# Kernel optimization log

Hardware: AMD Instinct MI355X
Metric: run time of the kernel (lower is better)

The kernel has to match this reference:

```python
import jax, jax.numpy as jnp
import numpy as np

C_Z = 128
N_HEADS = 4
HEAD_DIM = 32
TOTAL = N_HEADS * HEAD_DIM
B, N = 1, 256


def setup_inputs() -> dict:
    key = jax.random.key(0)
    ks = jax.random.split(key, 10)
    s = lambda k, sh: jax.random.normal(k, sh, dtype=jnp.float32) * 0.02
    return {
        "pair_representation": jax.random.normal(ks[0], (B, N, N, C_Z), dtype=jnp.float32),
        "ln_gamma": jnp.ones((C_Z,), jnp.float32),
        "ln_beta": jnp.zeros((C_Z,), jnp.float32),
        "Wq": s(ks[1], (C_Z, TOTAL)),
        "Wk": s(ks[2], (C_Z, TOTAL)),
        "Wv": s(ks[3], (C_Z, TOTAL)),
        "Wb": s(ks[4], (C_Z, N_HEADS)),
        "Wg": s(ks[5], (C_Z, TOTAL)),
        "bg": jnp.zeros((TOTAL,), jnp.float32),
        "Wo": s(ks[6], (TOTAL, C_Z)),
        "bo": jnp.zeros((C_Z,), jnp.float32),
    }


def reference(pair_representation, ln_gamma, ln_beta, Wq, Wk, Wv, Wb, Wg, bg, Wo, bo):
    x = pair_representation
    # LayerNorm over c_z
    mu = jnp.mean(x, axis=-1, keepdims=True)
    var = jnp.mean((x - mu) ** 2, axis=-1, keepdims=True)
    x = (x - mu) * jax.lax.rsqrt(var + 1e-5) * ln_gamma + ln_beta

    b, n, _, _ = x.shape
    split = lambda t: t.reshape(b, n, n, N_HEADS, HEAD_DIM)
    Q = split(x @ Wq)  # [b,i,j,h,d]
    K = split(x @ Wk)
    V = split(x @ Wv)
    G = jax.nn.sigmoid(split(x @ Wg + bg))
    Bias = x @ Wb  # [b,j,k,h]

    scores = jnp.einsum("bijhd,bikhd->bijkh", Q, K) / np.float32(np.sqrt(HEAD_DIM))
    scores = scores + Bias[:, None]  # broadcast over i
    attn = jax.nn.softmax(scores, axis=3)  # over k
    vals = jnp.einsum("bijkh,bikhd->bijhd", attn, V)
    vals = (G * vals).reshape(b, n, n, TOTAL)
    return vals @ Wo + bo
```

## Files before the change

### kernel.cpp

```cpp
#include <hip/hip_runtime.h>
#include <hip/hip_bf16.h>


#define QSCALE 0.17677669529663687f

typedef __attribute__((ext_vector_type(8))) short bf16x8;
typedef __attribute__((ext_vector_type(4))) short bf16x4;
typedef __attribute__((ext_vector_type(4))) float f32x4;

#define MFMA32(a, b, c) __builtin_amdgcn_mfma_f32_16x16x32_bf16((a), (b), (c), 0, 0, 0)

__device__ __forceinline__ f32x4 mfma16_asm(bf16x4 a, bf16x4 b, f32x4 c) {
    f32x4 d;
    asm volatile("v_mfma_f32_16x16x16_bf16 %0, %1, %2, %3"
                 : "=v"(d) : "v"(a), "v"(b), "v"(c));
    return d;
}

#if !defined(__HIP_DEVICE_COMPILE__)
#define MFMA16(a, b, c) (c)
#elif __has_builtin(__builtin_amdgcn_mfma_f32_16x16x16bf16_1k)
#define MFMA16(a, b, c) __builtin_amdgcn_mfma_f32_16x16x16bf16_1k((a), (b), (c), 0, 0, 0)
#else
#define MFMA16(a, b, c) mfma16_asm((a), (b), (c))
#endif

__device__ __forceinline__ ushort f2bf(float f) {
    uint32_t u = __builtin_bit_cast(uint32_t, f);
    uint32_t r = (u + 0x7FFFu + ((u >> 16) & 1u)) >> 16;
    return (ushort)r;
}
__device__ __forceinline__ uint pk2(float a, float b) {
    union { __hip_bfloat162 h; uint u; } cv;
    cv.h = __float22bfloat162_rn(make_float2(a, b));
    return cv.u;
}

__global__ __launch_bounds__(256) void prep_bias_kernel(
    const float* __restrict__ Wq, const float* __restrict__ Wk, const float* __restrict__ Wv,
    const float* __restrict__ Wg, const float* __restrict__ Wo, const float* __restrict__ Wb,
    const float* __restrict__ x, const float* __restrict__ gamma, const float* __restrict__ beta,
    ushort* __restrict__ Wfrag, ushort* __restrict__ WoFrag,
    ushort* __restrict__ xn, float* __restrict__ EbF)
{
    __shared__ float WbS[512];
    __shared__ float gS[128];
    __shared__ float bS[128];

    if (blockIdx.x < 320) {
        int idx = blockIdx.x * 256 + threadIdx.x;
        if (idx < 65536) {
            int j = idx & 7, lane = (idx >> 3) & 63, ks = (idx >> 9) & 3, ct = idx >> 11;
            int n = ct * 16 + (lane & 15);
            int k = ks * 32 + (lane >> 4) * 8 + j;
            float v;
            if (n < 128)      v = Wq[k * 128 + n] * QSCALE;
            else if (n < 256) v = Wk[k * 128 + (n - 128)];
            else if (n < 384) v = Wv[k * 128 + (n - 256)];
            else              v = Wg[k * 128 + (n - 384)];
            Wfrag[idx] = f2bf(v);
        } else {
            int idx2 = idx - 65536;
            int j = idx2 & 7, lane = (idx2 >> 3) & 63, ks = (idx2 >> 9) & 3, ct = idx2 >> 11;
            int n = ct * 16 + (lane & 15);
            int k = ks * 32 + (lane >> 4) * 8 + j;
            WoFrag[idx2] = f2bf(Wo[k * 128 + n]);
        }
        return;
    }

    const int t = threadIdx.x;
    if (t < 128)      { *(f32x4*)&WbS[t * 4] = *(const f32x4*)(Wb + t * 4); }
    else if (t < 160) { int c = (t - 128) * 4; *(f32x4*)&gS[c] = *(const f32x4*)(gamma + c); }
    else if (t < 192) { int c = (t - 160) * 4; *(f32x4*)&bS[c] = *(const f32x4*)(beta + c); }
    __syncthreads();

    const int wave = t >> 6, lane = t & 63, m = lane & 15, quad = lane >> 4;
    const int p = (blockIdx.x - 320) * 64 + wave * 16 + m;

    const float* rp0 = x + (size_t)p * 128;
    f32x4 xa[4][2];
    float sum = 0.f, ssq = 0.f;
#pragma unroll
    for (int ks = 0; ks < 4; ++ks) {
        xa[ks][0] = *(const f32x4*)(rp0 + ks * 32 + quad * 8);
        xa[ks][1] = *(const f32x4*)(rp0 + ks * 32 + quad * 8 + 4);
#pragma unroll
        for (int q4 = 0; q4 < 2; ++q4) {
            f32x4 v = xa[ks][q4];
            sum += v[0] + v[1] + v[2] + v[3];
            ssq += v[0]*v[0] + v[1]*v[1] + v[2]*v[2] + v[3]*v[3];
        }
    }
    sum += __shfl_xor(sum, 16); ssq += __shfl_xor(ssq, 16);
    sum += __shfl_xor(sum, 32); ssq += __shfl_xor(ssq, 32);
    const float mu   = sum * (1.f / 128.f);
    const float rstd = rsqrtf(ssq * (1.f / 128.f) - mu * mu + 1e-5f);

    float b0 = 0.f, b1 = 0.f, b2 = 0.f, b3 = 0.f;
#pragma unroll
    for (int ks = 0; ks < 4; ++ks) {
        uint4 pkd;
        uint pw[4];
#pragma unroll
        for (int q4 = 0; q4 < 2; ++q4) {
            const int c = ks * 32 + quad * 8 + q4 * 4;
            f32x4 v = xa[ks][q4];
            float n0 = (v[0] - mu) * rstd * gS[c + 0] + bS[c + 0];
            float n1 = (v[1] - mu) * rstd * gS[c + 1] + bS[c + 1];
            float n2 = (v[2] - mu) * rstd * gS[c + 2] + bS[c + 2];
            float n3 = (v[3] - mu) * rstd * gS[c + 3] + bS[c + 3];
            pw[q4 * 2]     = pk2(n0, n1);
            pw[q4 * 2 + 1] = pk2(n2, n3);
            f32x4 w0 = *(const f32x4*)&WbS[(c + 0) * 4];
            f32x4 w1 = *(const f32x4*)&WbS[(c + 1) * 4];
            f32x4 w2 = *(const f32x4*)&WbS[(c + 2) * 4];
            f32x4 w3 = *(const f32x4*)&WbS[(c + 3) * 4];
            b0 += n0*w0[0] + n1*w1[0] + n2*w2[0] + n3*w3[0];
            b1 += n0*w0[1] + n1*w1[1] + n2*w2[1] + n3*w3[1];
            b2 += n0*w0[2] + n1*w1[2] + n2*w2[2] + n3*w3[2];
            b3 += n0*w0[3] + n1*w1[3] + n2*w2[3] + n3*w3[3];
        }
        pkd.x = pw[0]; pkd.y = pw[1]; pkd.z = pw[2]; pkd.w = pw[3];
        *(uint4*)(xn + (size_t)p * 128 + ks * 32 + quad * 8) = pkd;
    }
    b0 += __shfl_xor(b0, 16); b1 += __shfl_xor(b1, 16); b2 += __shfl_xor(b2, 16); b3 += __shfl_xor(b3, 16);
    b0 += __shfl_xor(b0, 32); b1 += __shfl_xor(b1, 32); b2 += __shfl_xor(b2, 32); b3 += __shfl_xor(b3, 32);

    if (quad == 0) {
        const int row = p >> 8, col = p & 255;
        float bb[4] = {b0, b1, b2, b3};
#pragma unroll
        for (int r = 0; r < 4; ++r) {
            int addr = (((r * 16 + (row >> 4)) * 16 + (col >> 4)) * 64 +
                        ((col & 15) >> 2) * 16 + (row & 15)) * 4 + (col & 3);
            EbF[addr] = __expf(bb[r]);
        }
    }
}

__global__ __launch_bounds__(512, 1) void fused_kernel(
    const ushort* __restrict__ xn, const ushort* __restrict__ Wfrag,
    const float* __restrict__ bg, const float* __restrict__ EbF,
    const ushort* __restrict__ WoFrag, const float* __restrict__ bo,
    float* __restrict__ out)
{
    extern __shared__ __align__(16) ushort SM[];
    ushort* KL = SM;
    ushort* VT = SM + 32768;

    const f32x4 ZERO4 = {0.f, 0.f, 0.f, 0.f};

    const int t = threadIdx.x;
    const int w = t >> 6, lane = t & 63, m = lane & 15, quad = lane >> 4;
    const int i = blockIdx.x;
    const int h = w >> 1, half = w & 1;
    const int jbase = half * 128;
    const ushort* xb = xn + ((size_t)i << 15);

    {
        const ushort* Wm = Wfrag + (h * 2) * 2048;
        bf16x8 wfr[2][4];
#pragma unroll
        for (int ctl = 0; ctl < 2; ++ctl)
#pragma unroll
            for (int ks = 0; ks < 4; ++ks)
                wfr[ctl][ks] = *(const bf16x8*)(Wm + ctl * 2048 + ks * 512 + lane * 8);
#pragma unroll
        for (int grp = 0; grp < 8; ++grp) {
            const int jloc = grp * 16 + m;
            bf16x8 xg[4];
            const ushort* xp = xb + (size_t)(jbase + jloc) * 128 + quad * 8;
#pragma unroll
            for (int ks = 0; ks < 4; ++ks) xg[ks] = *(const bf16x8*)(xp + ks * 32);
#pragma unroll
            for (int ctl = 0; ctl < 2; ++ctl) {
                f32x4 acc = ZERO4;
#pragma unroll
                for (int ks = 0; ks < 4; ++ks) acc = MFMA32(wfr[ctl][ks], xg[ks], acc);
                const int c = ctl * 16 + quad * 4;
                const int idx = (w * 4096 + jloc * 32 + c) ^ ((jloc & 3) << 3);
                uint2 u; u.x = pk2(acc[0], acc[1]); u.y = pk2(acc[2], acc[3]);
                *(uint2*)(KL + idx) = u;
            }
        }
    }
    bf16x8 qf[8];
#pragma unroll
    for (int jt = 0; jt < 8; ++jt) {
        const int jloc = jt * 16 + m;
        const int idx = (w * 4096 + jloc * 32 + quad * 8) ^ ((jloc & 3) << 3);
        qf[jt] = *(const bf16x8*)(KL + idx);
    }
    asm volatile("" ::: "memory");

    {
        const ushort* Wm = Wfrag + (8 + h * 2) * 2048;
        bf16x8 wfr[2][4];
#pragma unroll
        for (int ctl = 0; ctl < 2; ++ctl)
#pragma unroll
            for (int ks = 0; ks < 4; ++ks)
                wfr[ctl][ks] = *(const bf16x8*)(Wm + ctl * 2048 + ks * 512 + lane * 8);
#pragma unroll
        for (int grp = 0; grp < 8; ++grp) {
            const int k = jbase + grp * 16 + m;
            bf16x8 xg[4];
            const ushort* xp = xb + (size_t)k * 128 + quad * 8;
#pragma unroll
            for (int ks = 0; ks < 4; ++ks) xg[ks] = *(const bf16x8*)(xp + ks * 32);
#pragma unroll
            for (int ctl = 0; ctl < 2; ++ctl) {
                f32x4 acc = ZERO4;
#pragma unroll
                for (int ks = 0; ks < 4; ++ks) acc = MFMA32(wfr[ctl][ks], xg[ks], acc);
                const int d0 = ctl * 16 + quad * 4;
                const int idx = (h * 8192 + (k >> 1) * 64 + (k & 1) * 32 + d0) ^ (((k >> 1) & 7) << 3);
                uint2 u; u.x = pk2(acc[0], acc[1]); u.y = pk2(acc[2], acc[3]);
                *(uint2*)(KL + idx) = u;
            }
        }
    }

    {
        const ushort* Wm = Wfrag + (16 + h * 2) * 2048;
        bf16x8 wfr[2][4];
#pragma unroll
        for (int ctl = 0; ctl < 2; ++ctl)
#pragma unroll
            for (int ks = 0; ks < 4; ++ks)
                wfr[ctl][ks] = *(const bf16x8*)(Wm + ctl * 2048 + ks * 512 + lane * 8);
#pragma unroll
        for (int grp = 0; grp < 8; ++grp) {
            const int k = jbase + grp * 16 + m;
            bf16x8 xg[4];
            const ushort* xp = xb + (size_t)k * 128 + quad * 8;
#pragma unroll
            for (int ks = 0; ks < 4; ++ks) xg[ks] = *(const bf16x8*)(xp + ks * 32);
#pragma unroll
            for (int ctl = 0; ctl < 2; ++ctl) {
                f32x4 acc = ZERO4;
#pragma unroll
                for (int ks = 0; ks < 4; ++ks) acc = MFMA32(wfr[ctl][ks], xg[ks], acc);
#pragma unroll
                for (int r = 0; r < 4; ++r) {
                    const int d = ctl * 16 + quad * 4 + r;
                    const int idx = ((h * 32 + d) * 256 + k) ^ ((d & 7) << 3);
                    VT[idx] = f2bf(acc[r]);
                }
            }
        }
    }
    __syncthreads();

    f32x4 O[8][2];
    float lsum[8];
#pragma unroll
    for (int jt = 0; jt < 8; ++jt) {
        O[jt][0] = ZERO4;
        O[jt][1] = ZERO4;
        lsum[jt] = 0.f;
    }
    const float* ebB = EbF + ((size_t)(h * 16 + half * 8) << 12) + (lane << 2);

    for (int kh = 0; kh < 16; ++kh) {
        f32x4 eb[8];
#pragma unroll
        for (int jt = 0; jt < 8; ++jt)
            eb[jt] = *(const f32x4*)(ebB + (jt << 12) + (kh << 8));
        const int k = kh * 16 + m;
        const int kidx = (h * 8192 + (k >> 1) * 64 + (k & 1) * 32 + quad * 8) ^ (((k >> 1) & 7) << 3);
        bf16x8 kf = *(const bf16x8*)(KL + kidx);
        bf16x4 vf[2];
#pragma unroll
        for (int dt = 0; dt < 2; ++dt) {
            const int d = dt * 16 + m;
            const int vidx = ((h * 32 + d) * 256 + kh * 16 + quad * 4) ^ ((d & 7) << 3);
            uint2 vv = *(const uint2*)(VT + vidx);
            vf[dt] = __builtin_bit_cast(bf16x4, vv);
        }
#pragma unroll
        for (int jt = 0; jt < 8; ++jt) {
            f32x4 S = MFMA32(kf, qf[jt], ZERO4);
            float p0 = __expf(S[0]) * eb[jt][0];
            float p1 = __expf(S[1]) * eb[jt][1];
            float p2 = __expf(S[2]) * eb[jt][2];
            float p3 = __expf(S[3]) * eb[jt][3];
            lsum[jt] += p0 + p1 + p2 + p3;
            uint2 pu; pu.x = pk2(p0, p1); pu.y = pk2(p2, p3);
            bf16x4 pf = __builtin_bit_cast(bf16x4, pu);
#pragma unroll
            for (int dt = 0; dt < 2; ++dt)
                O[jt][dt] = MFMA16(vf[dt], pf, O[jt][dt]);
        }
    }

#pragma unroll
    for (int jt = 0; jt < 8; ++jt) {
        float s = lsum[jt];
        s += __shfl_xor(s, 16);
        s += __shfl_xor(s, 32);
        lsum[jt] = 1.f / s;
    }

    uint2 gva[8][2];
    {
        const ushort* Wm = Wfrag + (24 + h * 2) * 2048;
        bf16x8 wfr[2][4];
        f32x4 bg4[2];
#pragma unroll
        for (int ctl = 0; ctl < 2; ++ctl) {
#pragma unroll
            for (int ks = 0; ks < 4; ++ks)
                wfr[ctl][ks] = *(const bf16x8*)(Wm + ctl * 2048 + ks * 512 + lane * 8);
            bg4[ctl] = *(const f32x4*)(bg + h * 32 + ctl * 16 + quad * 4);
        }
#pragma unroll
        for (int grp = 0; grp < 8; ++grp) {
            const float rl = lsum[grp];
            bf16x8 xg[4];
            const ushort* xp = xb + (size_t)(jbase + grp * 16 + m) * 128 + quad * 8;
#pragma unroll
            for (int ks = 0; ks < 4; ++ks) xg[ks] = *(const bf16x8*)(xp + ks * 32);
#pragma unroll
            for (int ctl = 0; ctl < 2; ++ctl) {
                f32x4 acc = ZERO4;
#pragma unroll
                for (int ks = 0; ks < 4; ++ks) acc = MFMA32(wfr[ctl][ks], xg[ks], acc);
                float g0 = 1.f / (1.f + __expf(-(acc[0] + bg4[ctl][0])));
                float g1 = 1.f / (1.f + __expf(-(acc[1] + bg4[ctl][1])));
                float g2 = 1.f / (1.f + __expf(-(acc[2] + bg4[ctl][2])));
                float g3 = 1.f / (1.f + __expf(-(acc[3] + bg4[ctl][3])));
                float v0 = O[grp][ctl][0] * rl * g0;
                float v1 = O[grp][ctl][1] * rl * g1;
                float v2 = O[grp][ctl][2] * rl * g2;
                float v3 = O[grp][ctl][3] * rl * g3;
                gva[grp][ctl].x = pk2(v0, v1);
                gva[grp][ctl].y = pk2(v2, v3);
            }
        }
    }
    __syncthreads();

#pragma unroll
    for (int grp = 0; grp < 8; ++grp) {
        const int j = jbase + grp * 16 + m;
#pragma unroll
        for (int ctl = 0; ctl < 2; ++ctl) {
            const int c0 = h * 32 + ctl * 16 + quad * 4;
            const int idx = (j * 128 + c0) ^ ((j & 7) << 3);
            *(uint2*)(KL + idx) = gva[grp][ctl];
        }
    }
    __syncthreads();

    bf16x8 gf[2][4];
#pragma unroll
    for (int grp = 0; grp < 2; ++grp) {
        const int pl = w * 32 + grp * 16 + m;
#pragma unroll
        for (int ks = 0; ks < 4; ++ks) {
            const int idx = (pl * 128 + ks * 32 + quad * 8) ^ ((pl & 7) << 3);
            gf[grp][ks] = *(const bf16x8*)(KL + idx);
        }
    }
#pragma unroll
    for (int ct = 0; ct < 8; ++ct) {
        bf16x8 wfr[4];
#pragma unroll
        for (int ks = 0; ks < 4; ++ks)
            wfr[ks] = *(const bf16x8*)(WoFrag + (ct * 4 + ks) * 512 + lane * 8);
        const int c0 = ct * 16 + quad * 4;
        f32x4 bov = *(const f32x4*)(bo + c0);
#pragma unroll
        for (int grp = 0; grp < 2; ++grp) {
            f32x4 acc = ZERO4;
#pragma unroll
            for (int ks = 0; ks < 4; ++ks) acc = MFMA32(wfr[ks], gf[grp][ks], acc);
            const int p = i * 256 + w * 32 + grp * 16 + m;
            float4 v = make_float4(acc[0] + bov[0], acc[1] + bov[1],
                                   acc[2] + bov[2], acc[3] + bov[3]);
            *(float4*)(out + (size_t)p * 128 + c0) = v;
        }
    }
}

extern "C" void kernel_launch(void* const* d_in, const int* in_sizes, int n_in,
                              void* d_out, int out_size, void* d_ws, size_t ws_size,
                              hipStream_t stream) {
    const float* x     = (const float*)d_in[0];
    const float* gamma = (const float*)d_in[1];
    const float* beta  = (const float*)d_in[2];
    const float* Wq    = (const float*)d_in[3];
    const float* Wk    = (const float*)d_in[4];
    const float* Wv    = (const float*)d_in[5];
    const float* Wb    = (const float*)d_in[6];
    const float* Wg    = (const float*)d_in[7];
    const float* bg    = (const float*)d_in[8];
    const float* Wo    = (const float*)d_in[9];
    const float* bo    = (const float*)d_in[10];

    ushort* ws      = (ushort*)d_ws;
    ushort* Wfrag   = ws;
    ushort* WoFragp = ws + 65536;
    ushort* xn      = ws + 81920;
    float*  EbF     = (float*)(ws + 81920 + 8388608);

    static bool attr_set = false;
    if (!attr_set) {
        (void)hipFuncSetAttribute((const void*)fused_kernel,
                                  hipFuncAttributeMaxDynamicSharedMemorySize, 131072);
        attr_set = true;
    }

    prep_bias_kernel<<<1344, 256, 0, stream>>>(Wq, Wk, Wv, Wg, Wo, Wb,
                                               x, gamma, beta,
                                               Wfrag, WoFragp, xn, EbF);
    fused_kernel<<<256, 512, 131072, stream>>>(xn, Wfrag, bg, EbF,
                                               WoFragp, bo, (float*)d_out);
}
```

Measured before the change: 162.5 us.

## Split fused attention block across 16 waves with quarter-row j tiles and prefetch bias

Doubles the block to 1024 threads so each head is handled by four waves covering 64 j-rows each instead of two waves covering 128. Per-wave register state (Q fragments, O accumulators, sums) is halved, and the exp(bias) tiles are software-prefetched one k-step ahead. The aim is more latency hiding and wave-level parallelism per CU. In exchange, each wave repeats the K/V fragment loads over fewer j-rows, and the launch bound (1024, 4) caps registers per thread.

```diff
diff --git a/kernel.cpp b/kernel.cpp
--- a/kernel.cpp
+++ b/kernel.cpp
@@ -139,7 +139,7 @@
     }
 }
 
-__global__ __launch_bounds__(512, 1) void fused_kernel(
+__global__ __launch_bounds__(1024, 4) void fused_kernel(
     const ushort* __restrict__ xn, const ushort* __restrict__ Wfrag,
     const float* __restrict__ bg, const float* __restrict__ EbF,
     const ushort* __restrict__ WoFrag, const float* __restrict__ bo,
@@ -154,8 +154,9 @@
     const int t = threadIdx.x;
     const int w = t >> 6, lane = t & 63, m = lane & 15, quad = lane >> 4;
     const int i = blockIdx.x;
-    const int h = w >> 1, half = w & 1;
-    const int jbase = half * 128;
+    const int h = w >> 2, quarter = w & 3;
+    const int jbase = quarter * 64;
+    const int qreg = h * 8192 + quarter * 2048;
     const ushort* xb = xn + ((size_t)i << 15);
 
     {
@@ -167,7 +168,7 @@
             for (int ks = 0; ks < 4; ++ks)
                 wfr[ctl][ks] = *(const bf16x8*)(Wm + ctl * 2048 + ks * 512 + lane * 8);
 #pragma unroll
-        for (int grp = 0; grp < 8; ++grp) {
+        for (int grp = 0; grp < 4; ++grp) {
             const int jloc = grp * 16 + m;
             bf16x8 xg[4];
             const ushort* xp = xb + (size_t)(jbase + jloc) * 128 + quad * 8;
@@ -179,17 +180,17 @@
 #pragma unroll
                 for (int ks = 0; ks < 4; ++ks) acc = MFMA32(wfr[ctl][ks], xg[ks], acc);
                 const int c = ctl * 16 + quad * 4;
-                const int idx = (w * 4096 + jloc * 32 + c) ^ ((jloc & 3) << 3);
+                const int idx = (qreg + jloc * 32 + c) ^ ((jloc & 3) << 3);
                 uint2 u; u.x = pk2(acc[0], acc[1]); u.y = pk2(acc[2], acc[3]);
                 *(uint2*)(KL + idx) = u;
             }
         }
     }
-    bf16x8 qf[8];
-#pragma unroll
-    for (int jt = 0; jt < 8; ++jt) {
+    bf16x8 qf[4];
+#pragma unroll
+    for (int jt = 0; jt < 4; ++jt) {
         const int jloc = jt * 16 + m;
-        const int idx = (w * 4096 + jloc * 32 + quad * 8) ^ ((jloc & 3) << 3);
+        const int idx = (qreg + jloc * 32 + quad * 8) ^ ((jloc & 3) << 3);
         qf[jt] = *(const bf16x8*)(KL + idx);
     }
     asm volatile("" ::: "memory");
@@ -203,7 +204,7 @@
             for (int ks = 0; ks < 4; ++ks)
                 wfr[ctl][ks] = *(const bf16x8*)(Wm + ctl * 2048 + ks * 512 + lane * 8);
 #pragma unroll
-        for (int grp = 0; grp < 8; ++grp) {
+        for (int grp = 0; grp < 4; ++grp) {
             const int k = jbase + grp * 16 + m;
             bf16x8 xg[4];
             const ushort* xp = xb + (size_t)k * 128 + quad * 8;
@@ -231,7 +232,7 @@
             for (int ks = 0; ks < 4; ++ks)
                 wfr[ctl][ks] = *(const bf16x8*)(Wm + ctl * 2048 + ks * 512 + lane * 8);
 #pragma unroll
-        for (int grp = 0; grp < 8; ++grp) {
+        for (int grp = 0; grp < 4; ++grp) {
             const int k = jbase + grp * 16 + m;
             bf16x8 xg[4];
             const ushort* xp = xb + (size_t)k * 128 + quad * 8;
@@ -253,21 +254,26 @@
     }
     __syncthreads();
 
-    f32x4 O[8][2];
-    float lsum[8];
-#pragma unroll
-    for (int jt = 0; jt < 8; ++jt) {
+    f32x4 O[4][2];
+    float lsum[4];
+#pragma unroll
+    for (int jt = 0; jt < 4; ++jt) {
         O[jt][0] = ZERO4;
         O[jt][1] = ZERO4;
         lsum[jt] = 0.f;
     }
-    const float* ebB = EbF + ((size_t)(h * 16 + half * 8) << 12) + (lane << 2);
+    const float* ebB = EbF + ((size_t)(h * 16 + quarter * 4) << 12) + (lane << 2);
+
+    f32x4 ebc[4], ebn[4];
+#pragma unroll
+    for (int jt = 0; jt < 4; ++jt) ebc[jt] = *(const f32x4*)(ebB + (jt << 12));
 
     for (int kh = 0; kh < 16; ++kh) {
-        f32x4 eb[8];
-#pragma unroll
-        for (int jt = 0; jt < 8; ++jt)
-            eb[jt] = *(const f32x4*)(ebB + (jt << 12) + (kh << 8));
+        if (kh < 15) {
+#pragma unroll
+            for (int jt = 0; jt < 4; ++jt)
+                ebn[jt] = *(const f32x4*)(ebB + (jt << 12) + ((kh + 1) << 8));
+        }
         const int k = kh * 16 + m;
         const int kidx = (h * 8192 + (k >> 1) * 64 + (k & 1) * 32 + quad * 8) ^ (((k >> 1) & 7) << 3);
         bf16x8 kf = *(const bf16x8*)(KL + kidx);
@@ -280,12 +286,12 @@
             vf[dt] = __builtin_bit_cast(bf16x4, vv);
         }
 #pragma unroll
-        for (int jt = 0; jt < 8; ++jt) {
+        for (int jt = 0; jt < 4; ++jt) {
             f32x4 S = MFMA32(kf, qf[jt], ZERO4);
-            float p0 = __expf(S[0]) * eb[jt][0];
-            float p1 = __expf(S[1]) * eb[jt][1];
-            float p2 = __expf(S[2]) * eb[jt][2];
-            float p3 = __expf(S[3]) * eb[jt][3];
+            float p0 = __expf(S[0]) * ebc[jt][0];
+            float p1 = __expf(S[1]) * ebc[jt][1];
+            float p2 = __expf(S[2]) * ebc[jt][2];
+            float p3 = __expf(S[3]) * ebc[jt][3];
             lsum[jt] += p0 + p1 + p2 + p3;
             uint2 pu; pu.x = pk2(p0, p1); pu.y = pk2(p2, p3);
             bf16x4 pf = __builtin_bit_cast(bf16x4, pu);
@@ -293,17 +299,19 @@
             for (int dt = 0; dt < 2; ++dt)
                 O[jt][dt] = MFMA16(vf[dt], pf, O[jt][dt]);
         }
-    }
-
-#pragma unroll
-    for (int jt = 0; jt < 8; ++jt) {
+#pragma unroll
+        for (int jt = 0; jt < 4; ++jt) ebc[jt] = ebn[jt];
+    }
+
+#pragma unroll
+    for (int jt = 0; jt < 4; ++jt) {
         float s = lsum[jt];
         s += __shfl_xor(s, 16);
         s += __shfl_xor(s, 32);
         lsum[jt] = 1.f / s;
     }
 
-    uint2 gva[8][2];
+    uint2 gva[4][2];
     {
         const ushort* Wm = Wfrag + (24 + h * 2) * 2048;
         bf16x8 wfr[2][4];
@@ -316,7 +324,7 @@
             bg4[ctl] = *(const f32x4*)(bg + h * 32 + ctl * 16 + quad * 4);
         }
 #pragma unroll
-        for (int grp = 0; grp < 8; ++grp) {
+        for (int grp = 0; grp < 4; ++grp) {
             const float rl = lsum[grp];
             bf16x8 xg[4];
             const ushort* xp = xb + (size_t)(jbase + grp * 16 + m) * 128 + quad * 8;
@@ -343,7 +351,7 @@
     __syncthreads();
 
 #pragma unroll
-    for (int grp = 0; grp < 8; ++grp) {
+    for (int grp = 0; grp < 4; ++grp) {
         const int j = jbase + grp * 16 + m;
 #pragma unroll
         for (int ctl = 0; ctl < 2; ++ctl) {
@@ -354,14 +362,13 @@
     }
     __syncthreads();
 
-    bf16x8 gf[2][4];
-#pragma unroll
-    for (int grp = 0; grp < 2; ++grp) {
-        const int pl = w * 32 + grp * 16 + m;
+    bf16x8 gf[4];
+    {
+        const int pl = w * 16 + m;
 #pragma unroll
         for (int ks = 0; ks < 4; ++ks) {
             const int idx = (pl * 128 + ks * 32 + quad * 8) ^ ((pl & 7) << 3);
-            gf[grp][ks] = *(const bf16x8*)(KL + idx);
+            gf[ks] = *(const bf16x8*)(KL + idx);
         }
     }
 #pragma unroll
@@ -372,16 +379,13 @@
             wfr[ks] = *(const bf16x8*)(WoFrag + (ct * 4 + ks) * 512 + lane * 8);
         const int c0 = ct * 16 + quad * 4;
         f32x4 bov = *(const f32x4*)(bo + c0);
-#pragma unroll
-        for (int grp = 0; grp < 2; ++grp) {
-            f32x4 acc = ZERO4;
-#pragma unroll
-            for (int ks = 0; ks < 4; ++ks) acc = MFMA32(wfr[ks], gf[grp][ks], acc);
-            const int p = i * 256 + w * 32 + grp * 16 + m;
-            float4 v = make_float4(acc[0] + bov[0], acc[1] + bov[1],
-                                   acc[2] + bov[2], acc[3] + bov[3]);
-            *(float4*)(out + (size_t)p * 128 + c0) = v;
-        }
+        f32x4 acc = ZERO4;
+#pragma unroll
+        for (int ks = 0; ks < 4; ++ks) acc = MFMA32(wfr[ks], gf[ks], acc);
+        const int p = i * 256 + w * 16 + m;
+        float4 v = make_float4(acc[0] + bov[0], acc[1] + bov[1],
+                               acc[2] + bov[2], acc[3] + bov[3]);
+        *(float4*)(out + (size_t)p * 128 + c0) = v;
     }
 }
 
@@ -416,6 +420,6 @@
     prep_bias_kernel<<<1344, 256, 0, stream>>>(Wq, Wk, Wv, Wg, Wo, Wb,
                                                x, gamma, beta,
                                                Wfrag, WoFragp, xn, EbF);
-    fused_kernel<<<256, 512, 131072, stream>>>(xn, Wfrag, bg, EbF,
-                                               WoFragp, bo, (float*)d_out);
-}
+    fused_kernel<<<256, 1024, 131072, stream>>>(xn, Wfrag, bg, EbF,
+                                                WoFragp, bo, (float*)d_out);
+}
```

Result: slower. 166.4 us (+2.4%).
